# Kernel optimization log

Measured on AMD Instinct MI355X. Metric: run time of the kernel, lower is better.

The kernel has to match this reference:

```python
import jax, jax.numpy as jnp
import numpy as np

N_USER = 50000
N_ITEM = 50000
E = 600000
D = 128   # in_channels per node type
H = 128   # hidden_channels


def setup_inputs() -> dict:
    key = jax.random.key(0)
    ks = jax.random.split(key, 11)
    wscale = 1.0 / np.sqrt(D)  # stand-in for glorot
    inp = {
        "x_user": jax.random.normal(ks[0], (N_USER, D), jnp.float32),
        "x_item": jax.random.normal(ks[1], (N_ITEM, D), jnp.float32),
        "w_rates_src": jax.random.normal(ks[2], (D, H), jnp.float32) * wscale,
        "w_rates_tgt": jax.random.normal(ks[3], (D, H), jnp.float32) * wscale,
        "w_rated_src": jax.random.normal(ks[4], (D, H), jnp.float32) * wscale,
        "w_rated_tgt": jax.random.normal(ks[5], (D, H), jnp.float32) * wscale,
        "w_follows_src": jax.random.normal(ks[6], (D, H), jnp.float32) * wscale,
        "w_follows_tgt": jax.random.normal(ks[7], (D, H), jnp.float32) * wscale,
        "edge_rates": jax.random.randint(ks[8], (2, E), 0, N_ITEM, jnp.int32),
        "edge_rated": jax.random.randint(ks[9], (2, E), 0, N_USER, jnp.int32),
        "edge_follows": jax.random.randint(ks[10], (2, E), 0, N_USER, jnp.int32),
    }
    return inp


def _segment_mean(vals, idx, num_segments):
    # scatter(..., reduce='mean') into zeros: untouched rows stay 0
    s = jax.ops.segment_sum(vals, idx, num_segments=num_segments)
    cnt = jax.ops.segment_sum(jnp.ones((idx.shape[0], 1), vals.dtype), idx,
                              num_segments=num_segments)
    return s / jnp.maximum(cnt, 1.0)


def _relation(x_src, x_tgt, w_src, w_tgt, edges, n_tgt):
    src_x = x_src @ w_src                      # [N_src, H]
    tgt_x = x_tgt @ w_tgt                      # [N_tgt, H]
    msg = src_x[edges[0]]                      # gather  [E, H]
    agg = _segment_mean(msg, edges[1], n_tgt)  # scatter-mean [N_tgt, H]
    return tgt_x + agg


def reference(x_user, x_item, w_rates_src, w_rates_tgt, w_rated_src,
              w_rated_tgt, w_follows_src, w_follows_tgt, edge_rates,
              edge_rated, edge_follows):
    # ('user','rates','item') -> target item
    out_item = _relation(x_user, x_item, w_rates_src, w_rates_tgt,
                         edge_rates, N_ITEM)
    # ('item','rated_by','user') -> target user
    out_user = _relation(x_item, x_user, w_rated_src, w_rated_tgt,
                         edge_rated, N_USER)
    # ('user','follows','user') -> target user (accumulated)
    out_user = out_user + _relation(x_user, x_user, w_follows_src,
                                    w_follows_tgt, edge_follows, N_USER)
    # divide by number of relations per target type, then double relu
    out_user = jax.nn.relu(jax.nn.relu(out_user / 2.0))
    out_item = jax.nn.relu(jax.nn.relu(out_item / 1.0))
    return out_user, out_item
```

## Files before the change

kernel.cpp:

```cpp
#include <hip/hip_runtime.h>
#include <hip/hip_bf16.h>

constexpr int NN = 50000;
constexpr int DD = 128;
constexpr int EE = 600000;
constexpr long long PP = (long long)NN * DD;
constexpr int NE3 = 3 * EE;
constexpr int BPR = (NN + 63) / 64;
constexpr int NBIN = 3 * BPR;
constexpr int NB = 512;
constexpr int CH = (NE3 + NB - 1) / NB;
constexpr int CAP = 2048;
constexpr float QSCALE = 4.0f / 127.0f;

typedef __bf16 bf16x8 __attribute__((ext_vector_type(8)));
typedef float f32x4 __attribute__((ext_vector_type(4)));

__device__ inline unsigned short f2bs(float x) {
    __hip_bfloat16 b = __float2bfloat16(x);
    return *reinterpret_cast<unsigned short*>(&b);
}
__device__ inline float bs2f(unsigned short u) {
    union { float f; unsigned int u; } x; x.u = ((unsigned int)u) << 16; return x.f;
}
__device__ inline unsigned char q8u(float x) {
    float c = fminf(fmaxf(x, -4.0f), 4.0f) * 31.75f;
    return (unsigned char)(__float2int_rn(c) + 128);
}

__global__ void cvtx_kernel(const float* __restrict__ xu, const float* __restrict__ xi,
                            unsigned short* __restrict__ xub, unsigned short* __restrict__ xib,
                            unsigned char* __restrict__ xu8, unsigned char* __restrict__ xi8) {
    const int total = (int)(PP / 4);
    for (int i = blockIdx.x * blockDim.x + threadIdx.x; i < total;
         i += gridDim.x * blockDim.x) {
        float4 a = ((const float4*)xu)[i];
        float4 b = ((const float4*)xi)[i];
        ushort4 oa, ob;
        oa.x = f2bs(a.x); oa.y = f2bs(a.y); oa.z = f2bs(a.z); oa.w = f2bs(a.w);
        ob.x = f2bs(b.x); ob.y = f2bs(b.y); ob.z = f2bs(b.z); ob.w = f2bs(b.w);
        ((ushort4*)xub)[i] = oa;
        ((ushort4*)xib)[i] = ob;
        uchar4 ca, cb;
        ca.x = q8u(a.x); ca.y = q8u(a.y); ca.z = q8u(a.z); ca.w = q8u(a.w);
        cb.x = q8u(b.x); cb.y = q8u(b.y); cb.z = q8u(b.z); cb.w = q8u(b.w);
        ((uchar4*)xu8)[i] = ca;
        ((uchar4*)xi8)[i] = cb;
    }
}

__global__ void wprep_kernel(const float* __restrict__ wrt, const float* __restrict__ wft,
                             const float* __restrict__ wrs, const float* __restrict__ wfs,
                             const float* __restrict__ wit, const float* __restrict__ wis,
                             unsigned short* __restrict__ Wu, unsigned short* __restrict__ Wi) {
    int n = blockIdx.x;
    for (int k = threadIdx.x; k < 384; k += blockDim.x) {
        int seg = k >> 7, ks = k & 127;
        float v = (seg == 0) ? (wrt[ks * 128 + n] + wft[ks * 128 + n])
                : (seg == 1) ? wrs[ks * 128 + n] : wfs[ks * 128 + n];
        Wu[n * 384 + k] = f2bs(v);
    }
    for (int k = threadIdx.x; k < 256; k += blockDim.x) {
        int seg = k >> 7, ks = k & 127;
        float v = (seg == 0) ? wit[ks * 128 + n] : wis[ks * 128 + n];
        Wi[n * 256 + k] = f2bs(v);
    }
}


__global__ __launch_bounds__(256) void bucket_hist_kernel(
    const int* __restrict__ t0, const int* __restrict__ t1,
    const int* __restrict__ t2, unsigned int* __restrict__ hist) {
    __shared__ unsigned int h[NBIN];
    for (int i = threadIdx.x; i < NBIN; i += 256) h[i] = 0;
    __syncthreads();
    const int start = blockIdx.x * CH;
    const int end = (start + CH < NE3) ? start + CH : NE3;
    for (int idx = start + threadIdx.x; idx < end; idx += 256) {
        int rel = idx / EE;
        int e = idx - rel * EE;
        const int* tp = (rel == 0) ? t0 : (rel == 1) ? t1 : t2;
        atomicAdd(&h[rel * BPR + (tp[e] >> 6)], 1u);
    }
    __syncthreads();
    for (int i = threadIdx.x; i < NBIN; i += 256)
        hist[(size_t)blockIdx.x * NBIN + i] = h[i];
}

__global__ void bucket_base_kernel(const unsigned int* __restrict__ hist,
                                   unsigned int* __restrict__ base,
                                   unsigned int* __restrict__ bintot) {
    int bin = blockIdx.x * blockDim.x + threadIdx.x;
    if (bin >= NBIN) return;
    unsigned int run = 0;
    for (int b = 0; b < NB; ++b) {
        unsigned int v = hist[(size_t)b * NBIN + bin];
        base[(size_t)b * NBIN + bin] = run;
        run += v;
    }
    bintot[bin] = run;
}

__global__ __launch_bounds__(256) void scan_part_kernel(
    const int* __restrict__ cnt, int* __restrict__ rowst,
    int* __restrict__ bsum, int n) {
    const int tid = threadIdx.x;
    const int base = blockIdx.x * 4096 + tid * 16;
    int v[16];
    #pragma unroll
    for (int i = 0; i < 16; ++i) {
        int g = base + i;
        v[i] = (g < n) ? cnt[g] : 0;
    }
    int s = 0;
    #pragma unroll
    for (int i = 0; i < 16; ++i) s += v[i];
    const int lane = tid & 63, wv = tid >> 6;
    int incl = s;
    #pragma unroll
    for (int d = 1; d < 64; d <<= 1) {
        int u = __shfl_up(incl, d, 64);
        if (lane >= d) incl += u;
    }
    __shared__ int wsum[4];
    if (lane == 63) wsum[wv] = incl;
    __syncthreads();
    int woff = 0;
    for (int w = 0; w < wv; ++w) woff += wsum[w];
    int run = woff + incl - s;
    #pragma unroll
    for (int i = 0; i < 16; ++i) {
        int g = base + i;
        if (g < n) rowst[g] = run;
        run += v[i];
    }
    if (tid == 255) bsum[blockIdx.x] = woff + incl;
}

__global__ __launch_bounds__(256) void bucket_scatter_kernel(
    const int* __restrict__ s0, const int* __restrict__ t0,
    const int* __restrict__ s1, const int* __restrict__ t1,
    const int* __restrict__ s2, const int* __restrict__ t2,
    const unsigned int* __restrict__ base, const int* __restrict__ bkstart,
    unsigned int* __restrict__ bucketed) {
    __shared__ unsigned int cur[NBIN];
    for (int i = threadIdx.x; i < NBIN; i += 256)
        cur[i] = (unsigned int)bkstart[i] + base[(size_t)blockIdx.x * NBIN + i];
    __syncthreads();
    const int start = blockIdx.x * CH;
    const int end = (start + CH < NE3) ? start + CH : NE3;
    for (int idx = start + threadIdx.x; idx < end; idx += 256) {
        int rel = idx / EE;
        int e = idx - rel * EE;
        const int* tp = (rel == 0) ? t0 : (rel == 1) ? t1 : t2;
        const int* sp = (rel == 0) ? s0 : (rel == 1) ? s1 : s2;
        int t = tp[e];
        unsigned int pos = atomicAdd(&cur[rel * BPR + (t >> 6)], 1u);
        bucketed[pos] = ((unsigned int)(t & 63) << 16) | (unsigned int)sp[e];
    }
}

__global__ __launch_bounds__(256) void bucket_gather_kernel(
    const unsigned char* __restrict__ xu8, const unsigned char* __restrict__ xi8,
    const int* __restrict__ bkstart, const unsigned int* __restrict__ bucketed,
    unsigned short* __restrict__ accb) {
    __shared__ unsigned int raw[CAP];
    __shared__ unsigned short sorted[CAP];
    __shared__ unsigned int fcnt[64], fstart[64], cursor[64];

    const int b = blockIdx.x;
    const int rel = b / BPR;
    const int tb = (b - rel * BPR) * 64;
    const unsigned char* srcm = (rel == 0) ? xi8 : xu8;
    const int start = bkstart[b];
    const int end = (b == NBIN - 1) ? NE3 : bkstart[b + 1];

    const int tid = threadIdx.x;
    const int grp = tid >> 4;
    const int l = tid & 15;

    unsigned int s[4][4];
    int deg[4] = {0, 0, 0, 0};
    #pragma unroll
    for (int q = 0; q < 4; ++q)
        #pragma unroll
        for (int k = 0; k < 4; ++k) s[q][k] = 0u;

    for (int c0 = start; c0 < end; c0 += CAP) {
        const int n = (end - c0 < CAP) ? end - c0 : CAP;
        if (tid < 64) fcnt[tid] = 0;
        __syncthreads();
        for (int i = tid; i < n; i += 256) {
            unsigned int r = bucketed[c0 + i];
            raw[i] = r;
            atomicAdd(&fcnt[r >> 16], 1u);
        }
        __syncthreads();
        if (tid < 64) {
            unsigned int v = fcnt[tid];
            unsigned int incl = v;
            #pragma unroll
            for (int d = 1; d < 64; d <<= 1) {
                unsigned int u = __shfl_up(incl, d, 64);
                if ((tid & 63) >= d) incl += u;
            }
            fstart[tid] = incl - v;
            cursor[tid] = incl - v;
        }
        __syncthreads();
        for (int i = tid; i < n; i += 256) {
            unsigned int r = raw[i];
            unsigned int pos = atomicAdd(&cursor[r >> 16], 1u);
            sorted[pos] = (unsigned short)r;
        }
        __syncthreads();

        #pragma unroll
        for (int q = 0; q < 4; ++q) {
            const int f = grp + 16 * q;
            const int cf = (int)fcnt[f];
            const int st = (int)fstart[f];
            deg[q] += cf;
            int j = 0;
            for (; j + 4 <= cf; j += 4) {
                int sa = sorted[st + j];
                int sb = sorted[st + j + 1];
                int sc = sorted[st + j + 2];
                int sd = sorted[st + j + 3];
                uint2 va = *(const uint2*)(srcm + (size_t)sa * DD + l * 8);
                uint2 vb = *(const uint2*)(srcm + (size_t)sb * DD + l * 8);
                uint2 vc = *(const uint2*)(srcm + (size_t)sc * DD + l * 8);
                uint2 vd = *(const uint2*)(srcm + (size_t)sd * DD + l * 8);
                s[q][0] += (va.x & 0x00FF00FFu) + (vb.x & 0x00FF00FFu)
                         + (vc.x & 0x00FF00FFu) + (vd.x & 0x00FF00FFu);
                s[q][1] += ((va.x >> 8) & 0x00FF00FFu) + ((vb.x >> 8) & 0x00FF00FFu)
                         + ((vc.x >> 8) & 0x00FF00FFu) + ((vd.x >> 8) & 0x00FF00FFu);
                s[q][2] += (va.y & 0x00FF00FFu) + (vb.y & 0x00FF00FFu)
                         + (vc.y & 0x00FF00FFu) + (vd.y & 0x00FF00FFu);
                s[q][3] += ((va.y >> 8) & 0x00FF00FFu) + ((vb.y >> 8) & 0x00FF00FFu)
                         + ((vc.y >> 8) & 0x00FF00FFu) + ((vd.y >> 8) & 0x00FF00FFu);
            }
            for (; j < cf; ++j) {
                int sa = sorted[st + j];
                uint2 va = *(const uint2*)(srcm + (size_t)sa * DD + l * 8);
                s[q][0] += (va.x & 0x00FF00FFu);
                s[q][1] += ((va.x >> 8) & 0x00FF00FFu);
                s[q][2] += (va.y & 0x00FF00FFu);
                s[q][3] += ((va.y >> 8) & 0x00FF00FFu);
            }
        }
        __syncthreads();
    }

    #pragma unroll
    for (int q = 0; q < 4; ++q) {
        const int f = grp + 16 * q;
        const int t = tb + f;
        if (t < NN) {
            float bias = 128.0f * (float)deg[q];
            float inv = QSCALE / (float)(deg[q] > 1 ? deg[q] : 1);
            float m[8];
            m[0] = ((float)(s[q][0] & 0xFFFFu) - bias) * inv;
            m[2] = ((float)(s[q][0] >> 16)    - bias) * inv;
            m[1] = ((float)(s[q][1] & 0xFFFFu) - bias) * inv;
            m[3] = ((float)(s[q][1] >> 16)    - bias) * inv;
            m[4] = ((float)(s[q][2] & 0xFFFFu) - bias) * inv;
            m[6] = ((float)(s[q][2] >> 16)    - bias) * inv;
            m[5] = ((float)(s[q][3] & 0xFFFFu) - bias) * inv;
            m[7] = ((float)(s[q][3] >> 16)    - bias) * inv;
            uint4 o;
            o.x = ((unsigned int)f2bs(m[1]) << 16) | f2bs(m[0]);
            o.y = ((unsigned int)f2bs(m[3]) << 16) | f2bs(m[2]);
            o.z = ((unsigned int)f2bs(m[5]) << 16) | f2bs(m[4]);
            o.w = ((unsigned int)f2bs(m[7]) << 16) | f2bs(m[6]);
            *(uint4*)(accb + (size_t)(rel * NN + t) * DD + l * 8) = o;
        }
    }
}

__device__ __forceinline__ void gemm_body(
    const unsigned short* __restrict__ a0, const unsigned short* __restrict__ a1,
    const unsigned short* __restrict__ a2, const unsigned short* __restrict__ Wt,
    float* __restrict__ outp, float postmul, int ksteps,
    unsigned char* lAb, unsigned char* lBb) {
    const int tid = threadIdx.x;
    const int m0 = blockIdx.x * 64;
    const int Ktot = ksteps * 64;
    const int wv = tid >> 6, lane = tid & 63;
    const int rbase = tid >> 4;
    const int ku = tid & 15;

    f32x4 acc[8];
    #pragma unroll
    for (int j = 0; j < 8; ++j) acc[j] = (f32x4)(0.f);

    unsigned long long aReg[4], bReg[8];
    #pragma unroll
    for (int i = 0; i < 4; ++i) {
        int g = m0 + rbase + i * 16;
        aReg[i] = (g < NN)
            ? *(const unsigned long long*)(a0 + (size_t)g * DD + ku * 4) : 0ull;
    }
    #pragma unroll
    for (int i = 0; i < 8; ++i) {
        int n = rbase + i * 16;
        bReg[i] = *(const unsigned long long*)(Wt + (size_t)n * Ktot + ku * 4);
    }

    for (int kt = 0; kt < ksteps; ++kt) {
        #pragma unroll
        for (int i = 0; i < 4; ++i) {
            int row = rbase + i * 16;
            int byte = (row * 128 + ku * 8) ^ ((row & 7) << 4);
            *(unsigned long long*)(lAb + byte) = aReg[i];
        }
        #pragma unroll
        for (int i = 0; i < 8; ++i) {
            int n = rbase + i * 16;
            int byte = (n * 128 + ku * 8) ^ ((n & 7) << 4);
            *(unsigned long long*)(lBb + byte) = bReg[i];
        }
        __syncthreads();

        if (kt + 1 < ksteps) {
            const int ktn = kt + 1;
            const unsigned short* As = (ktn >> 1) == 0 ? a0
                                     : (ktn >> 1) == 1 ? a1 : a2;
            const int ks0 = (ktn & 1) * 64;
            #pragma unroll
            for (int i = 0; i < 4; ++i) {
                int g = m0 + rbase + i * 16;
                aReg[i] = (g < NN)
                    ? *(const unsigned long long*)(As + (size_t)g * DD + ks0 + ku * 4)
                    : 0ull;
            }
            #pragma unroll
            for (int i = 0; i < 8; ++i) {
                int n = rbase + i * 16;
                bReg[i] = *(const unsigned long long*)(
                    Wt + (size_t)n * Ktot + ktn * 64 + ku * 4);
            }
        }

        #pragma unroll
        for (int kk = 0; kk < 2; ++kk) {
            int row = wv * 16 + (lane & 15);
            int abyte = (row * 128 + kk * 64 + (lane >> 4) * 16) ^ ((row & 7) << 4);
            bf16x8 af = *(const bf16x8*)(lAb + abyte);
            #pragma unroll
            for (int ni = 0; ni < 8; ++ni) {
                int n = ni * 16 + (lane & 15);
                int byte = (n * 128 + kk * 64 + (lane >> 4) * 16) ^ ((n & 7) << 4);
                bf16x8 bfr = *(const bf16x8*)(lBb + byte);
                acc[ni] = __builtin_amdgcn_mfma_f32_16x16x32_bf16(
                    af, bfr, acc[ni], 0, 0, 0);
            }
        }
        __syncthreads();
    }

    #pragma unroll
    for (int ni = 0; ni < 8; ++ni) {
        #pragma unroll
        for (int r = 0; r < 4; ++r) {
            int g = m0 + wv * 16 + (lane >> 4) * 4 + r;
            if (g < NN) {
                float v = acc[ni][r] * postmul;
                outp[(size_t)g * DD + ni * 16 + (lane & 15)] = v > 0.f ? v : 0.f;
            }
        }
    }
}

__global__ __launch_bounds__(256) void mfma_gemm2_kernel(
    const unsigned short* __restrict__ xub, const unsigned short* __restrict__ xib,
    const unsigned short* __restrict__ accb, const unsigned short* __restrict__ Wu,
    const unsigned short* __restrict__ Wi, float* __restrict__ out_user,
    float* __restrict__ out_item) {
    __shared__ unsigned char lAb[64 * 128];
    __shared__ unsigned char lBb[128 * 128];
    if (blockIdx.y == 0)
        gemm_body(xub, accb, accb + PP, Wu, out_user, 0.5f, 6, lAb, lBb);
    else
        gemm_body(xib, accb + 2 * PP, nullptr, Wi, out_item, 1.0f, 4, lAb, lBb);
}

extern "C" void kernel_launch(void* const* d_in, const int* in_sizes, int n_in,
                              void* d_out, int out_size, void* d_ws, size_t ws_size,
                              hipStream_t stream) {
    const float* x_user = (const float*)d_in[0];
    const float* x_item = (const float*)d_in[1];
    const float* w_rates_src   = (const float*)d_in[2];
    const float* w_rates_tgt   = (const float*)d_in[3];
    const float* w_rated_src   = (const float*)d_in[4];
    const float* w_rated_tgt   = (const float*)d_in[5];
    const float* w_follows_src = (const float*)d_in[6];
    const float* w_follows_tgt = (const float*)d_in[7];
    const int* e_rates   = (const int*)d_in[8];
    const int* e_rated   = (const int*)d_in[9];
    const int* e_follows = (const int*)d_in[10];

    char* p = (char*)d_ws;
    unsigned short* xub  = (unsigned short*)p; p += (size_t)PP * 2;
    unsigned short* xib  = (unsigned short*)p; p += (size_t)PP * 2;
    unsigned char* xu8   = (unsigned char*)p; p += (size_t)PP;
    unsigned char* xi8   = (unsigned char*)p; p += (size_t)PP;
    unsigned short* accb = (unsigned short*)p; p += (size_t)3 * PP * 2;
    unsigned short* Wu   = (unsigned short*)p; p += (size_t)128 * 384 * 2;
    unsigned short* Wi   = (unsigned short*)p; p += (size_t)128 * 256 * 2;
    unsigned int* bintot = (unsigned int*)p; p += (size_t)NBIN * 4;
    int* bkstart         = (int*)p; p += (size_t)(NBIN + 64) * 4;
    int* bsum            = (int*)p; p += (size_t)64 * 4;
    unsigned int* bucketed = (unsigned int*)p; p += (size_t)NE3 * 4;

    unsigned int* hist = (unsigned int*)accb;
    unsigned int* base = hist + (size_t)NB * NBIN;

    float* out_user = (float*)d_out;
    float* out_item = out_user + PP;

    cvtx_kernel<<<2048, 256, 0, stream>>>(x_user, x_item, xub, xib, xu8, xi8);
    wprep_kernel<<<128, 256, 0, stream>>>(w_rated_tgt, w_follows_tgt, w_rated_src,
                                          w_follows_src, w_rates_tgt, w_rates_src,
                                          Wu, Wi);
    bucket_hist_kernel<<<NB, 256, 0, stream>>>(e_rated + EE, e_follows + EE,
                                               e_rates + EE, hist);
    bucket_base_kernel<<<(NBIN + 255) / 256, 256, 0, stream>>>(hist, base, bintot);
    scan_part_kernel<<<1, 256, 0, stream>>>((const int*)bintot, bkstart, bsum, NBIN);
    bucket_scatter_kernel<<<NB, 256, 0, stream>>>(e_rated, e_rated + EE,
                                                  e_follows, e_follows + EE,
                                                  e_rates, e_rates + EE,
                                                  base, bkstart, bucketed);
    bucket_gather_kernel<<<NBIN, 256, 0, stream>>>(xu8, xi8, bkstart, bucketed, accb);

    dim3 gg((NN + 63) / 64, 2);
    mfma_gemm2_kernel<<<gg, 256, 0, stream>>>(xub, xib, accb, Wu, Wi,
                                              out_user, out_item);
}
```

Measured before the change: 148.1 us.

## Double-buffer LDS and prefetch two k-steps ahead in MFMA GEMM

Turns the GEMM k-loop into a double-buffered LDS pipeline. Global loads for step kt+2 go into a second register set and the LDS write for step kt+1 goes into the other buffer, so each iteration needs one barrier instead of two. The k-step count becomes a template parameter so the loop can be fully unrolled. In exchange, LDS use doubles to 48KB per block and register pressure grows, which may lower occupancy.

```diff
diff --git a/kernel.cpp b/kernel.cpp
--- a/kernel.cpp
+++ b/kernel.cpp
@@ -278,14 +278,15 @@
     }
 }
 
+template<int KSTEPS>
 __device__ __forceinline__ void gemm_body(
     const unsigned short* __restrict__ a0, const unsigned short* __restrict__ a1,
     const unsigned short* __restrict__ a2, const unsigned short* __restrict__ Wt,
-    float* __restrict__ outp, float postmul, int ksteps,
-    unsigned char* lAb, unsigned char* lBb) {
+    float* __restrict__ outp, float postmul,
+    unsigned char* lA, unsigned char* lB) {
     const int tid = threadIdx.x;
     const int m0 = blockIdx.x * 64;
-    const int Ktot = ksteps * 64;
+    const int Ktot = KSTEPS * 64;
     const int wv = tid >> 6, lane = tid & 63;
     const int rbase = tid >> 4;
     const int ku = tid & 15;
@@ -294,68 +295,69 @@
     #pragma unroll
     for (int j = 0; j < 8; ++j) acc[j] = (f32x4)(0.f);
 
-    unsigned long long aReg[4], bReg[8];
-    #pragma unroll
-    for (int i = 0; i < 4; ++i) {
-        int g = m0 + rbase + i * 16;
-        aReg[i] = (g < NN)
-            ? *(const unsigned long long*)(a0 + (size_t)g * DD + ku * 4) : 0ull;
-    }
-    #pragma unroll
-    for (int i = 0; i < 8; ++i) {
-        int n = rbase + i * 16;
-        bReg[i] = *(const unsigned long long*)(Wt + (size_t)n * Ktot + ku * 4);
-    }
-
-    for (int kt = 0; kt < ksteps; ++kt) {
+    unsigned long long aR[2][4], bR[2][8];
+
+    auto loadRegs = [&](int kt, int set) {
+        const unsigned short* As = (kt >> 1) == 0 ? a0 : (kt >> 1) == 1 ? a1 : a2;
+        const int ks0 = (kt & 1) * 64;
+        #pragma unroll
+        for (int i = 0; i < 4; ++i) {
+            int g = m0 + rbase + i * 16;
+            aR[set][i] = (g < NN)
+                ? *(const unsigned long long*)(As + (size_t)g * DD + ks0 + ku * 4)
+                : 0ull;
+        }
+        #pragma unroll
+        for (int i = 0; i < 8; ++i) {
+            int n = rbase + i * 16;
+            bR[set][i] = *(const unsigned long long*)(
+                Wt + (size_t)n * Ktot + kt * 64 + ku * 4);
+        }
+    };
+    auto writeLds = [&](int buf, int set) {
+        unsigned char* la = lA + buf * 64 * 128;
+        unsigned char* lb = lB + buf * 128 * 128;
         #pragma unroll
         for (int i = 0; i < 4; ++i) {
             int row = rbase + i * 16;
             int byte = (row * 128 + ku * 8) ^ ((row & 7) << 4);
-            *(unsigned long long*)(lAb + byte) = aReg[i];
+            *(unsigned long long*)(la + byte) = aR[set][i];
         }
         #pragma unroll
         for (int i = 0; i < 8; ++i) {
             int n = rbase + i * 16;
             int byte = (n * 128 + ku * 8) ^ ((n & 7) << 4);
-            *(unsigned long long*)(lBb + byte) = bReg[i];
-        }
-        __syncthreads();
-
-        if (kt + 1 < ksteps) {
-            const int ktn = kt + 1;
-            const unsigned short* As = (ktn >> 1) == 0 ? a0
-                                     : (ktn >> 1) == 1 ? a1 : a2;
-            const int ks0 = (ktn & 1) * 64;
-            #pragma unroll
-            for (int i = 0; i < 4; ++i) {
-                int g = m0 + rbase + i * 16;
-                aReg[i] = (g < NN)
-                    ? *(const unsigned long long*)(As + (size_t)g * DD + ks0 + ku * 4)
-                    : 0ull;
-            }
-            #pragma unroll
-            for (int i = 0; i < 8; ++i) {
-                int n = rbase + i * 16;
-                bReg[i] = *(const unsigned long long*)(
-                    Wt + (size_t)n * Ktot + ktn * 64 + ku * 4);
-            }
-        }
-
+            *(unsigned long long*)(lb + byte) = bR[set][i];
+        }
+    };
+
+    loadRegs(0, 0);
+    writeLds(0, 0);
+    if (KSTEPS > 1) loadRegs(1, 1);
+    __syncthreads();
+
+    #pragma unroll
+    for (int kt = 0; kt < KSTEPS; ++kt) {
+        const int cb = kt & 1;
+        if (kt + 2 < KSTEPS) loadRegs(kt + 2, cb);
+
+        unsigned char* la = lA + cb * 64 * 128;
+        unsigned char* lb = lB + cb * 128 * 128;
         #pragma unroll
         for (int kk = 0; kk < 2; ++kk) {
             int row = wv * 16 + (lane & 15);
             int abyte = (row * 128 + kk * 64 + (lane >> 4) * 16) ^ ((row & 7) << 4);
-            bf16x8 af = *(const bf16x8*)(lAb + abyte);
+            bf16x8 af = *(const bf16x8*)(la + abyte);
             #pragma unroll
             for (int ni = 0; ni < 8; ++ni) {
                 int n = ni * 16 + (lane & 15);
                 int byte = (n * 128 + kk * 64 + (lane >> 4) * 16) ^ ((n & 7) << 4);
-                bf16x8 bfr = *(const bf16x8*)(lBb + byte);
+                bf16x8 bfr = *(const bf16x8*)(lb + byte);
                 acc[ni] = __builtin_amdgcn_mfma_f32_16x16x32_bf16(
                     af, bfr, acc[ni], 0, 0, 0);
             }
         }
+        if (kt + 1 < KSTEPS) writeLds((kt + 1) & 1, (kt + 1) & 1);
         __syncthreads();
     }
 
@@ -377,12 +379,12 @@
     const unsigned short* __restrict__ accb, const unsigned short* __restrict__ Wu,
     const unsigned short* __restrict__ Wi, float* __restrict__ out_user,
     float* __restrict__ out_item) {
-    __shared__ unsigned char lAb[64 * 128];
-    __shared__ unsigned char lBb[128 * 128];
+    __shared__ unsigned char lA[2 * 64 * 128];
+    __shared__ unsigned char lB[2 * 128 * 128];
     if (blockIdx.y == 0)
-        gemm_body(xub, accb, accb + PP, Wu, out_user, 0.5f, 6, lAb, lBb);
+        gemm_body<6>(xub, accb, accb + PP, Wu, out_user, 0.5f, lA, lB);
     else
-        gemm_body(xib, accb + 2 * PP, nullptr, Wi, out_item, 1.0f, 4, lAb, lBb);
+        gemm_body<4>(xib, accb + 2 * PP, nullptr, Wi, out_item, 1.0f, lA, lB);
 }
 
 extern "C" void kernel_launch(void* const* d_in, const int* in_sizes, int n_in,
```

Result: no change. 150.7 us (+1.8%).
